# Kernel tuning notes

Measured on AMD Instinct MI355X. Metric: run time of the kernel, lower is better.

Reference implementation:

```python
import jax, jax.numpy as jnp
import numpy as np

B, S, D, H = 4, 2048, 768, 12
HD = D // H  # head dim = 64


def setup_inputs() -> dict:
    key = jax.random.key(0)
    ks = jax.random.split(key, 8)
    w_scale = 0.02
    return {
        "x": jax.random.normal(ks[0], (B, S, D), dtype=jnp.float32),
        "Wq": jax.random.normal(ks[1], (D, D), dtype=jnp.float32) * w_scale,
        "bq": jnp.zeros((D,), dtype=jnp.float32),
        "Wk": jax.random.normal(ks[2], (D, D), dtype=jnp.float32) * w_scale,
        "Wv": jax.random.normal(ks[3], (D, D), dtype=jnp.float32) * w_scale,
        "bv": jnp.zeros((D,), dtype=jnp.float32),
        "Wo": jax.random.normal(ks[4], (D, D), dtype=jnp.float32) * w_scale,
        "bo": jnp.zeros((D,), dtype=jnp.float32),
    }


def reference(x, Wq, bq, Wk, Wv, bv, Wo, bo):
    # Self-attention branch (xa=None, no kv_cache), causal mask enabled.
    q = x @ Wq + bq                       # [B,S,D]; key proj has no bias
    k = x @ Wk
    v = x @ Wv + bv

    def split_heads(t):
        return t.reshape(B, S, H, HD).transpose(0, 2, 1, 3)  # [B,H,S,HD]

    q, k, v = split_heads(q), split_heads(k), split_heads(v)

    scale = float(HD) ** -0.5  # applied once to qk == (hd**-0.25 on q and k)
    qk = jnp.einsum("bhqd,bhkd->bhqk", q, k) * scale  # [B,H,S,S]

    # dynamic causal mask: -inf where kv index > q index
    causal = jnp.where(
        jnp.arange(S)[:, None] < jnp.arange(S)[None, :], -jnp.inf, 0.0
    ).astype(jnp.float32)
    qk = qk + causal

    w = jax.nn.softmax(qk.astype(jnp.float32), axis=-1).astype(q.dtype)
    out = jnp.einsum("bhqk,bhkd->bhqd", w, v)          # [B,H,S,HD]
    out = out.transpose(0, 2, 1, 3).reshape(B, S, D)    # [B,S,D]
    output = out @ Wo + bo
    return output, jax.lax.stop_gradient(qk)
```

## Files before the change

kernel.cpp:

```cpp
#include <hip/hip_runtime.h>
#include <cmath>

#define BB 4
#define SS 2048
#define DD 768
#define HH 12
#define HDD 64
#define MROWS (BB * SS)
#define NHEADS (BB * HH)

#define MASK_SENTINEL (-3.0e38f)

template <bool SPLIT_HEADS>
__global__ __launch_bounds__(256) void gemm768(const float* __restrict__ A,
                                               const float* __restrict__ W,
                                               const float* __restrict__ bias,
                                               float* __restrict__ out) {
    __shared__ float As[16][68];
    __shared__ float Bs[16][68];

    const int tid = threadIdx.x;
    const int tx = tid & 15;
    const int ty = tid >> 4;
    const int m0 = blockIdx.y * 64;
    const int n0 = blockIdx.x * 64;

    const int ar = tid >> 2;
    const int ac4 = (tid & 3) * 4;
    const int br = tid >> 4;
    const int bc4 = (tid & 15) * 4;

    float acc[4][4] = {};

    for (int k0 = 0; k0 < 768; k0 += 16) {
        if (k0 != 0) __syncthreads();
        const float4 av = *reinterpret_cast<const float4*>(
            &A[(size_t)(m0 + ar) * 768 + k0 + ac4]);
        As[ac4 + 0][ar] = av.x;
        As[ac4 + 1][ar] = av.y;
        As[ac4 + 2][ar] = av.z;
        As[ac4 + 3][ar] = av.w;
        *reinterpret_cast<float4*>(&Bs[br][bc4]) =
            *reinterpret_cast<const float4*>(&W[(size_t)(k0 + br) * 768 + n0 + bc4]);
        __syncthreads();

#pragma unroll
        for (int kk = 0; kk < 16; ++kk) {
            const float4 a = *reinterpret_cast<const float4*>(&As[kk][ty * 4]);
            const float4 b = *reinterpret_cast<const float4*>(&Bs[kk][tx * 4]);
            const float af[4] = {a.x, a.y, a.z, a.w};
            const float bf[4] = {b.x, b.y, b.z, b.w};
#pragma unroll
            for (int i = 0; i < 4; ++i)
#pragma unroll
                for (int j = 0; j < 4; ++j)
                    acc[i][j] = fmaf(af[i], bf[j], acc[i][j]);
        }
    }

#pragma unroll
    for (int i = 0; i < 4; ++i) {
        const int m = m0 + ty * 4 + i;
#pragma unroll
        for (int j = 0; j < 4; ++j) {
            const int n = n0 + tx * 4 + j;
            float v = acc[i][j];
            if (bias != nullptr) v += bias[n];
            if (SPLIT_HEADS) {
                const int b = m >> 11;
                const int s = m & 2047;
                const int h = n >> 6;
                const int hd = n & 63;
                out[(((size_t)(b * HH + h)) * SS + s) * HDD + hd] = v;
            } else {
                out[(size_t)m * 768 + n] = v;
            }
        }
    }
}

__global__ __launch_bounds__(256) void attn_flash(const float* __restrict__ q,
                                                  const float* __restrict__ k,
                                                  const float* __restrict__ v,
                                                  float* __restrict__ qk_out,
                                                  float* __restrict__ attn_out) {
    __shared__ float Ks[64][68];
    __shared__ float Vs[64][68];

    const int tid = threadIdx.x;
    const int quarter = tid & 3;
    const int row = tid >> 2;
    const int pair = blockIdx.x;
    const int bh = blockIdx.y;
    const size_t head_base = (size_t)bh * SS * HDD;
    const float scale = 0.125f;
    const int b_idx = bh / HH;
    const int h_idx = bh % HH;

    const int sr = tid >> 2;
    const int scb = (tid & 3) * 16;

#pragma unroll 1
    for (int leg = 0; leg < 2; ++leg) {
        const int tq = (leg == 0) ? (31 - pair) : pair;
        const int q0 = tq * 64;
        const int qr = q0 + row;

        float4 qreg[4];
        {
            const float* qp = q + head_base + (size_t)qr * HDD + quarter * 16;
#pragma unroll
            for (int c = 0; c < 4; ++c)
                qreg[c] = reinterpret_cast<const float4*>(qp)[c];
        }

        float4 o[4];
#pragma unroll
        for (int c = 0; c < 4; ++c) o[c] = make_float4(0.f, 0.f, 0.f, 0.f);
        float m_i = -INFINITY;
        float l_i = 0.0f;

        float* qk_row = qk_out + ((size_t)bh * SS + qr) * SS;

        const int kt_end = tq + 1;

        for (int kt = 0; kt < kt_end; ++kt) {
            __syncthreads();
            {
                const float* kp = k + head_base + (size_t)(kt * 64 + sr) * HDD + scb;
                const float* vp = v + head_base + (size_t)(kt * 64 + sr) * HDD + scb;
#pragma unroll
                for (int i = 0; i < 4; ++i) {
                    *reinterpret_cast<float4*>(&Ks[sr][scb + i * 4]) =
                        reinterpret_cast<const float4*>(kp)[i];
                    *reinterpret_cast<float4*>(&Vs[sr][scb + i * 4]) =
                        reinterpret_cast<const float4*>(vp)[i];
                }
            }
            __syncthreads();

            for (int jc = 0; jc < 64; jc += 16) {
                float sreg[16];
#pragma unroll
                for (int jj = 0; jj < 16; ++jj) {
                    const int j = jc + jj;
                    float acc = 0.f;
#pragma unroll
                    for (int c = 0; c < 4; ++c) {
                        const float4 kv = *reinterpret_cast<const float4*>(
                            &Ks[j][quarter * 16 + c * 4]);
                        acc = fmaf(qreg[c].x, kv.x, acc);
                        acc = fmaf(qreg[c].y, kv.y, acc);
                        acc = fmaf(qreg[c].z, kv.z, acc);
                        acc = fmaf(qreg[c].w, kv.w, acc);
                    }
                    acc += __shfl_xor(acc, 1);
                    acc += __shfl_xor(acc, 2);
                    const int jg = kt * 64 + j;
                    sreg[jj] = (jg > qr) ? -INFINITY : acc * scale;
                }

                {
                    const float w0 = fmaxf(sreg[quarter * 4 + 0], MASK_SENTINEL);
                    const float w1 = fmaxf(sreg[quarter * 4 + 1], MASK_SENTINEL);
                    const float w2 = fmaxf(sreg[quarter * 4 + 2], MASK_SENTINEL);
                    const float w3 = fmaxf(sreg[quarter * 4 + 3], MASK_SENTINEL);
                    *reinterpret_cast<float4*>(&qk_row[kt * 64 + jc + quarter * 4]) =
                        make_float4(w0, w1, w2, w3);
                }

                float mc = sreg[0];
#pragma unroll
                for (int jj = 1; jj < 16; ++jj) mc = fmaxf(mc, sreg[jj]);
                const float m_new = fmaxf(m_i, mc);
                if (m_new != -INFINITY) {
                    const float alpha = __expf(m_i - m_new);
                    float psum = 0.f;
#pragma unroll
                    for (int jj = 0; jj < 16; ++jj) {
                        sreg[jj] = __expf(sreg[jj] - m_new);
                        psum += sreg[jj];
                    }
                    l_i = l_i * alpha + psum;
                    m_i = m_new;
#pragma unroll
                    for (int c = 0; c < 4; ++c) {
                        o[c].x *= alpha;
                        o[c].y *= alpha;
                        o[c].z *= alpha;
                        o[c].w *= alpha;
                    }
#pragma unroll
                    for (int jj = 0; jj < 16; ++jj) {
                        const float p = sreg[jj];
#pragma unroll
                        for (int c = 0; c < 4; ++c) {
                            const float4 vv = *reinterpret_cast<const float4*>(
                                &Vs[jc + jj][quarter * 16 + c * 4]);
                            o[c].x = fmaf(p, vv.x, o[c].x);
                            o[c].y = fmaf(p, vv.y, o[c].y);
                            o[c].z = fmaf(p, vv.z, o[c].z);
                            o[c].w = fmaf(p, vv.w, o[c].w);
                        }
                    }
                }
            }
        }

        const float4 sent4 = make_float4(MASK_SENTINEL, MASK_SENTINEL,
                                         MASK_SENTINEL, MASK_SENTINEL);
        for (int base = kt_end * 64; base < SS; base += 16)
            *reinterpret_cast<float4*>(&qk_row[base + quarter * 4]) = sent4;

        const float inv_l = 1.0f / l_i;
        float* op = attn_out + ((size_t)(b_idx * SS + qr)) * DD + h_idx * HDD +
                    quarter * 16;
#pragma unroll
        for (int c = 0; c < 4; ++c) {
            float4 t = o[c];
            t.x *= inv_l;
            t.y *= inv_l;
            t.z *= inv_l;
            t.w *= inv_l;
            reinterpret_cast<float4*>(op)[c] = t;
        }
    }
}

extern "C" void kernel_launch(void* const* d_in, const int* in_sizes, int n_in,
                              void* d_out, int out_size, void* d_ws, size_t ws_size,
                              hipStream_t stream) {
    const float* x = (const float*)d_in[0];
    const float* Wq = (const float*)d_in[1];
    const float* bq = (const float*)d_in[2];
    const float* Wk = (const float*)d_in[3];
    const float* Wv = (const float*)d_in[4];
    const float* bv = (const float*)d_in[5];
    const float* Wo = (const float*)d_in[6];
    const float* bo = (const float*)d_in[7];

    float* out = (float*)d_out;
    float* qk = out + (size_t)BB * SS * DD;

    const size_t seg = (size_t)BB * SS * DD;
    float* qws = (float*)d_ws;
    float* kws = qws + seg;
    float* vws = qws + 2 * seg;
    float* aws = qws + 3 * seg;

    const dim3 gblk(256);
    const dim3 ggrid(DD / 64, MROWS / 64);

    gemm768<true><<<ggrid, gblk, 0, stream>>>(x, Wq, bq, qws);
    gemm768<true><<<ggrid, gblk, 0, stream>>>(x, Wk, nullptr, kws);
    gemm768<true><<<ggrid, gblk, 0, stream>>>(x, Wv, bv, vws);

    attn_flash<<<dim3(16, NHEADS), dim3(256), 0, stream>>>(qws, kws, vws, qk, aws);

    gemm768<false><<<ggrid, gblk, 0, stream>>>(aws, Wo, bo, out);
}
```

Measured before the change: 2.251 ms.

## Enlarge GEMM register tiles and give each attention thread two query rows

The projection GEMM moves to 128x64 block tiles with an 8x8 register tile per thread, 128 threads per block, register-staged global loads and vectorized epilogue stores. The attention kernel now has each thread handle two query rows over an 8-wide slice of the head dimension, so each K/V shared-memory read is reused for two rows. It also prefetches K/V into registers before the barrier, uses non-temporal stores for the large qk output, and replaces the dead-row branch with selects. Larger per-thread tiles raise register pressure and may reduce occupancy, and the wider shuffle reduction adds a step per score.

```diff
diff --git a/kernel.cpp b/kernel.cpp
--- a/kernel.cpp
+++ b/kernel.cpp
@@ -11,70 +11,92 @@
 
 #define MASK_SENTINEL (-3.0e38f)
 
+typedef float f32x4v __attribute__((ext_vector_type(4)));
+
+__device__ __forceinline__ void nt_store4(float* p, float a, float b, float c,
+                                          float d) {
+    f32x4v t = {a, b, c, d};
+    __builtin_nontemporal_store(t, reinterpret_cast<f32x4v*>(p));
+}
+
 template <bool SPLIT_HEADS>
-__global__ __launch_bounds__(256) void gemm768(const float* __restrict__ A,
+__global__ __launch_bounds__(128) void gemm768(const float* __restrict__ A,
                                                const float* __restrict__ W,
                                                const float* __restrict__ bias,
                                                float* __restrict__ out) {
-    __shared__ float As[16][68];
+    __shared__ float As[16][132];
     __shared__ float Bs[16][68];
 
     const int tid = threadIdx.x;
-    const int tx = tid & 15;
-    const int ty = tid >> 4;
-    const int m0 = blockIdx.y * 64;
+    const int tx = tid & 7;
+    const int ty = tid >> 3;
+    const int m0 = blockIdx.y * 128;
     const int n0 = blockIdx.x * 64;
 
-    const int ar = tid >> 2;
-    const int ac4 = (tid & 3) * 4;
-    const int br = tid >> 4;
-    const int bc4 = (tid & 15) * 4;
-
-    float acc[4][4] = {};
+    const int br = tid >> 3;
+    const int bc = (tid & 7) * 8;
+
+    float acc[8][8] = {};
 
     for (int k0 = 0; k0 < 768; k0 += 16) {
+        float4 av[4];
+        const float* ap = &A[(size_t)(m0 + tid) * 768 + k0];
+#pragma unroll
+        for (int c = 0; c < 4; ++c) av[c] = reinterpret_cast<const float4*>(ap)[c];
+        float4 bv[2];
+        const float* bp = &W[(size_t)(k0 + br) * 768 + n0 + bc];
+        bv[0] = reinterpret_cast<const float4*>(bp)[0];
+        bv[1] = reinterpret_cast<const float4*>(bp)[1];
+
         if (k0 != 0) __syncthreads();
-        const float4 av = *reinterpret_cast<const float4*>(
-            &A[(size_t)(m0 + ar) * 768 + k0 + ac4]);
-        As[ac4 + 0][ar] = av.x;
-        As[ac4 + 1][ar] = av.y;
-        As[ac4 + 2][ar] = av.z;
-        As[ac4 + 3][ar] = av.w;
-        *reinterpret_cast<float4*>(&Bs[br][bc4]) =
-            *reinterpret_cast<const float4*>(&W[(size_t)(k0 + br) * 768 + n0 + bc4]);
+#pragma unroll
+        for (int c = 0; c < 4; ++c) {
+            As[c * 4 + 0][tid] = av[c].x;
+            As[c * 4 + 1][tid] = av[c].y;
+            As[c * 4 + 2][tid] = av[c].z;
+            As[c * 4 + 3][tid] = av[c].w;
+        }
+        *reinterpret_cast<float4*>(&Bs[br][bc]) = bv[0];
+        *reinterpret_cast<float4*>(&Bs[br][bc + 4]) = bv[1];
         __syncthreads();
 
 #pragma unroll
         for (int kk = 0; kk < 16; ++kk) {
-            const float4 a = *reinterpret_cast<const float4*>(&As[kk][ty * 4]);
-            const float4 b = *reinterpret_cast<const float4*>(&Bs[kk][tx * 4]);
-            const float af[4] = {a.x, a.y, a.z, a.w};
-            const float bf[4] = {b.x, b.y, b.z, b.w};
-#pragma unroll
-            for (int i = 0; i < 4; ++i)
-#pragma unroll
-                for (int j = 0; j < 4; ++j)
+            const float4 a0 = *reinterpret_cast<const float4*>(&As[kk][ty * 8]);
+            const float4 a1 = *reinterpret_cast<const float4*>(&As[kk][ty * 8 + 4]);
+            const float4 b0 = *reinterpret_cast<const float4*>(&Bs[kk][tx * 8]);
+            const float4 b1 = *reinterpret_cast<const float4*>(&Bs[kk][tx * 8 + 4]);
+            const float af[8] = {a0.x, a0.y, a0.z, a0.w, a1.x, a1.y, a1.z, a1.w};
+            const float bf[8] = {b0.x, b0.y, b0.z, b0.w, b1.x, b1.y, b1.z, b1.w};
+#pragma unroll
+            for (int i = 0; i < 8; ++i)
+#pragma unroll
+                for (int j = 0; j < 8; ++j)
                     acc[i][j] = fmaf(af[i], bf[j], acc[i][j]);
         }
     }
 
-#pragma unroll
-    for (int i = 0; i < 4; ++i) {
-        const int m = m0 + ty * 4 + i;
-#pragma unroll
-        for (int j = 0; j < 4; ++j) {
-            const int n = n0 + tx * 4 + j;
-            float v = acc[i][j];
-            if (bias != nullptr) v += bias[n];
-            if (SPLIT_HEADS) {
-                const int b = m >> 11;
-                const int s = m & 2047;
-                const int h = n >> 6;
-                const int hd = n & 63;
-                out[(((size_t)(b * HH + h)) * SS + s) * HDD + hd] = v;
-            } else {
-                out[(size_t)m * 768 + n] = v;
-            }
+    float bn[8];
+#pragma unroll
+    for (int j = 0; j < 8; ++j) bn[j] = (bias != nullptr) ? bias[n0 + tx * 8 + j] : 0.f;
+
+    const int h = n0 >> 6;
+#pragma unroll
+    for (int i = 0; i < 8; ++i) {
+        const int m = m0 + ty * 8 + i;
+        float r[8];
+#pragma unroll
+        for (int j = 0; j < 8; ++j) r[j] = acc[i][j] + bn[j];
+        if (SPLIT_HEADS) {
+            const int b = m >> 11;
+            const int s = m & 2047;
+            float* op = &out[(((size_t)(b * HH + h)) * SS + s) * HDD + tx * 8];
+            *reinterpret_cast<float4*>(op) = make_float4(r[0], r[1], r[2], r[3]);
+            *reinterpret_cast<float4*>(op + 4) = make_float4(r[4], r[5], r[6], r[7]);
+        } else {
+            float* op = &out[(size_t)m * 768 + n0 + tx * 8];
+            *reinterpret_cast<float4*>(op) = make_float4(r[0], r[1], r[2], r[3]);
+            *reinterpret_cast<float4*>(op + 4) = make_float4(r[4], r[5], r[6], r[7]);
         }
     }
 }
@@ -88,8 +110,9 @@
     __shared__ float Vs[64][68];
 
     const int tid = threadIdx.x;
-    const int quarter = tid & 3;
-    const int row = tid >> 2;
+    const int oct = tid & 7;
+    const int rg = (tid >> 3) & 31;
+    const int d0 = oct * 8;
     const int pair = blockIdx.x;
     const int bh = blockIdx.y;
     const size_t head_base = (size_t)bh * SS * HDD;
@@ -100,129 +123,190 @@
     const int sr = tid >> 2;
     const int scb = (tid & 3) * 16;
 
+    const int rsel = oct >> 2;
+    const int g = oct & 3;
+
 #pragma unroll 1
     for (int leg = 0; leg < 2; ++leg) {
         const int tq = (leg == 0) ? (31 - pair) : pair;
         const int q0 = tq * 64;
-        const int qr = q0 + row;
-
-        float4 qreg[4];
+        const int qr0 = q0 + rg;
+        const int qr1 = q0 + rg + 32;
+
+        float4 q0reg[2], q1reg[2];
         {
-            const float* qp = q + head_base + (size_t)qr * HDD + quarter * 16;
-#pragma unroll
-            for (int c = 0; c < 4; ++c)
-                qreg[c] = reinterpret_cast<const float4*>(qp)[c];
-        }
-
-        float4 o[4];
-#pragma unroll
-        for (int c = 0; c < 4; ++c) o[c] = make_float4(0.f, 0.f, 0.f, 0.f);
-        float m_i = -INFINITY;
-        float l_i = 0.0f;
-
-        float* qk_row = qk_out + ((size_t)bh * SS + qr) * SS;
+            const float* qp0 = q + head_base + (size_t)qr0 * HDD + d0;
+            const float* qp1 = q + head_base + (size_t)qr1 * HDD + d0;
+            q0reg[0] = reinterpret_cast<const float4*>(qp0)[0];
+            q0reg[1] = reinterpret_cast<const float4*>(qp0)[1];
+            q1reg[0] = reinterpret_cast<const float4*>(qp1)[0];
+            q1reg[1] = reinterpret_cast<const float4*>(qp1)[1];
+        }
+
+        float4 o0[2], o1[2];
+#pragma unroll
+        for (int c = 0; c < 2; ++c) {
+            o0[c] = make_float4(0.f, 0.f, 0.f, 0.f);
+            o1[c] = make_float4(0.f, 0.f, 0.f, 0.f);
+        }
+        float m0i = -INFINITY, l0 = 0.f;
+        float m1i = -INFINITY, l1 = 0.f;
+
+        float* qk_row0 = qk_out + ((size_t)bh * SS + qr0) * SS;
+        float* qk_row1 = qk_out + ((size_t)bh * SS + qr1) * SS;
 
         const int kt_end = tq + 1;
 
         for (int kt = 0; kt < kt_end; ++kt) {
-            __syncthreads();
+            float4 kreg[4], vreg[4];
             {
                 const float* kp = k + head_base + (size_t)(kt * 64 + sr) * HDD + scb;
                 const float* vp = v + head_base + (size_t)(kt * 64 + sr) * HDD + scb;
 #pragma unroll
                 for (int i = 0; i < 4; ++i) {
-                    *reinterpret_cast<float4*>(&Ks[sr][scb + i * 4]) =
-                        reinterpret_cast<const float4*>(kp)[i];
-                    *reinterpret_cast<float4*>(&Vs[sr][scb + i * 4]) =
-                        reinterpret_cast<const float4*>(vp)[i];
+                    kreg[i] = reinterpret_cast<const float4*>(kp)[i];
+                    vreg[i] = reinterpret_cast<const float4*>(vp)[i];
                 }
             }
             __syncthreads();
+#pragma unroll
+            for (int i = 0; i < 4; ++i) {
+                *reinterpret_cast<float4*>(&Ks[sr][scb + i * 4]) = kreg[i];
+                *reinterpret_cast<float4*>(&Vs[sr][scb + i * 4]) = vreg[i];
+            }
+            __syncthreads();
 
             for (int jc = 0; jc < 64; jc += 16) {
-                float sreg[16];
+                float s0[16], s1[16];
 #pragma unroll
                 for (int jj = 0; jj < 16; ++jj) {
                     const int j = jc + jj;
-                    float acc = 0.f;
-#pragma unroll
-                    for (int c = 0; c < 4; ++c) {
-                        const float4 kv = *reinterpret_cast<const float4*>(
-                            &Ks[j][quarter * 16 + c * 4]);
-                        acc = fmaf(qreg[c].x, kv.x, acc);
-                        acc = fmaf(qreg[c].y, kv.y, acc);
-                        acc = fmaf(qreg[c].z, kv.z, acc);
-                        acc = fmaf(qreg[c].w, kv.w, acc);
+                    const float4 kv0 = *reinterpret_cast<const float4*>(&Ks[j][d0]);
+                    const float4 kv1 =
+                        *reinterpret_cast<const float4*>(&Ks[j][d0 + 4]);
+                    float a0 = 0.f, a1 = 0.f;
+                    a0 = fmaf(q0reg[0].x, kv0.x, a0);
+                    a0 = fmaf(q0reg[0].y, kv0.y, a0);
+                    a0 = fmaf(q0reg[0].z, kv0.z, a0);
+                    a0 = fmaf(q0reg[0].w, kv0.w, a0);
+                    a0 = fmaf(q0reg[1].x, kv1.x, a0);
+                    a0 = fmaf(q0reg[1].y, kv1.y, a0);
+                    a0 = fmaf(q0reg[1].z, kv1.z, a0);
+                    a0 = fmaf(q0reg[1].w, kv1.w, a0);
+                    a1 = fmaf(q1reg[0].x, kv0.x, a1);
+                    a1 = fmaf(q1reg[0].y, kv0.y, a1);
+                    a1 = fmaf(q1reg[0].z, kv0.z, a1);
+                    a1 = fmaf(q1reg[0].w, kv0.w, a1);
+                    a1 = fmaf(q1reg[1].x, kv1.x, a1);
+                    a1 = fmaf(q1reg[1].y, kv1.y, a1);
+                    a1 = fmaf(q1reg[1].z, kv1.z, a1);
+                    a1 = fmaf(q1reg[1].w, kv1.w, a1);
+                    a0 += __shfl_xor(a0, 1);
+                    a0 += __shfl_xor(a0, 2);
+                    a0 += __shfl_xor(a0, 4);
+                    a1 += __shfl_xor(a1, 1);
+                    a1 += __shfl_xor(a1, 2);
+                    a1 += __shfl_xor(a1, 4);
+                    const int jg = kt * 64 + j;
+                    s0[jj] = (jg > qr0) ? -INFINITY : a0 * scale;
+                    s1[jj] = (jg > qr1) ? -INFINITY : a1 * scale;
+                }
+
+                {
+                    float w[4];
+#pragma unroll
+                    for (int t = 0; t < 4; ++t) {
+                        const float x01 = (g & 1) ? s0[4 + t] : s0[t];
+                        const float x23 = (g & 1) ? s0[12 + t] : s0[8 + t];
+                        const float xs = (g & 2) ? x23 : x01;
+                        const float y01 = (g & 1) ? s1[4 + t] : s1[t];
+                        const float y23 = (g & 1) ? s1[12 + t] : s1[8 + t];
+                        const float ys = (g & 2) ? y23 : y01;
+                        w[t] = fmaxf(rsel ? ys : xs, MASK_SENTINEL);
                     }
-                    acc += __shfl_xor(acc, 1);
-                    acc += __shfl_xor(acc, 2);
-                    const int jg = kt * 64 + j;
-                    sreg[jj] = (jg > qr) ? -INFINITY : acc * scale;
-                }
-
-                {
-                    const float w0 = fmaxf(sreg[quarter * 4 + 0], MASK_SENTINEL);
-                    const float w1 = fmaxf(sreg[quarter * 4 + 1], MASK_SENTINEL);
-                    const float w2 = fmaxf(sreg[quarter * 4 + 2], MASK_SENTINEL);
-                    const float w3 = fmaxf(sreg[quarter * 4 + 3], MASK_SENTINEL);
-                    *reinterpret_cast<float4*>(&qk_row[kt * 64 + jc + quarter * 4]) =
-                        make_float4(w0, w1, w2, w3);
-                }
-
-                float mc = sreg[0];
-#pragma unroll
-                for (int jj = 1; jj < 16; ++jj) mc = fmaxf(mc, sreg[jj]);
-                const float m_new = fmaxf(m_i, mc);
-                if (m_new != -INFINITY) {
-                    const float alpha = __expf(m_i - m_new);
-                    float psum = 0.f;
-#pragma unroll
-                    for (int jj = 0; jj < 16; ++jj) {
-                        sreg[jj] = __expf(sreg[jj] - m_new);
-                        psum += sreg[jj];
-                    }
-                    l_i = l_i * alpha + psum;
-                    m_i = m_new;
-#pragma unroll
-                    for (int c = 0; c < 4; ++c) {
-                        o[c].x *= alpha;
-                        o[c].y *= alpha;
-                        o[c].z *= alpha;
-                        o[c].w *= alpha;
-                    }
-#pragma unroll
-                    for (int jj = 0; jj < 16; ++jj) {
-                        const float p = sreg[jj];
-#pragma unroll
-                        for (int c = 0; c < 4; ++c) {
-                            const float4 vv = *reinterpret_cast<const float4*>(
-                                &Vs[jc + jj][quarter * 16 + c * 4]);
-                            o[c].x = fmaf(p, vv.x, o[c].x);
-                            o[c].y = fmaf(p, vv.y, o[c].y);
-                            o[c].z = fmaf(p, vv.z, o[c].z);
-                            o[c].w = fmaf(p, vv.w, o[c].w);
-                        }
-                    }
+                    float* dst = (rsel ? qk_row1 : qk_row0) + kt * 64 + jc + g * 4;
+                    nt_store4(dst, w[0], w[1], w[2], w[3]);
+                }
+
+                float mc0 = s0[0], mc1 = s1[0];
+#pragma unroll
+                for (int jj = 1; jj < 16; ++jj) {
+                    mc0 = fmaxf(mc0, s0[jj]);
+                    mc1 = fmaxf(mc1, s1[jj]);
+                }
+                const float mn0 = fmaxf(m0i, mc0);
+                const float mn1 = fmaxf(m1i, mc1);
+                const bool dead0 = (mn0 == -INFINITY);
+                const bool dead1 = (mn1 == -INFINITY);
+                const float alpha0 = dead0 ? 1.f : __expf(m0i - mn0);
+                const float alpha1 = dead1 ? 1.f : __expf(m1i - mn1);
+                const float sub0 = dead0 ? 0.f : mn0;
+                const float sub1 = dead1 ? 0.f : mn1;
+                m0i = mn0;
+                m1i = mn1;
+                float ps0 = 0.f, ps1 = 0.f;
+#pragma unroll
+                for (int jj = 0; jj < 16; ++jj) {
+                    s0[jj] = __expf(s0[jj] - sub0);
+                    s1[jj] = __expf(s1[jj] - sub1);
+                    ps0 += s0[jj];
+                    ps1 += s1[jj];
+                }
+                l0 = l0 * alpha0 + ps0;
+                l1 = l1 * alpha1 + ps1;
+#pragma unroll
+                for (int c = 0; c < 2; ++c) {
+                    o0[c].x *= alpha0; o0[c].y *= alpha0;
+                    o0[c].z *= alpha0; o0[c].w *= alpha0;
+                    o1[c].x *= alpha1; o1[c].y *= alpha1;
+                    o1[c].z *= alpha1; o1[c].w *= alpha1;
+                }
+#pragma unroll
+                for (int jj = 0; jj < 16; ++jj) {
+                    const float4 vv0 =
+                        *reinterpret_cast<const float4*>(&Vs[jc + jj][d0]);
+                    const float4 vv1 =
+                        *reinterpret_cast<const float4*>(&Vs[jc + jj][d0 + 4]);
+                    const float p0 = s0[jj];
+                    const float p1 = s1[jj];
+                    o0[0].x = fmaf(p0, vv0.x, o0[0].x);
+                    o0[0].y = fmaf(p0, vv0.y, o0[0].y);
+                    o0[0].z = fmaf(p0, vv0.z, o0[0].z);
+                    o0[0].w = fmaf(p0, vv0.w, o0[0].w);
+                    o0[1].x = fmaf(p0, vv1.x, o0[1].x);
+                    o0[1].y = fmaf(p0, vv1.y, o0[1].y);
+                    o0[1].z = fmaf(p0, vv1.z, o0[1].z);
+                    o0[1].w = fmaf(p0, vv1.w, o0[1].w);
+                    o1[0].x = fmaf(p1, vv0.x, o1[0].x);
+                    o1[0].y = fmaf(p1, vv0.y, o1[0].y);
+                    o1[0].z = fmaf(p1, vv0.z, o1[0].z);
+                    o1[0].w = fmaf(p1, vv0.w, o1[0].w);
+                    o1[1].x = fmaf(p1, vv1.x, o1[1].x);
+                    o1[1].y = fmaf(p1, vv1.y, o1[1].y);
+                    o1[1].z = fmaf(p1, vv1.z, o1[1].z);
+                    o1[1].w = fmaf(p1, vv1.w, o1[1].w);
                 }
             }
         }
 
-        const float4 sent4 = make_float4(MASK_SENTINEL, MASK_SENTINEL,
-                                         MASK_SENTINEL, MASK_SENTINEL);
-        for (int base = kt_end * 64; base < SS; base += 16)
-            *reinterpret_cast<float4*>(&qk_row[base + quarter * 4]) = sent4;
-
-        const float inv_l = 1.0f / l_i;
-        float* op = attn_out + ((size_t)(b_idx * SS + qr)) * DD + h_idx * HDD +
-                    quarter * 16;
-#pragma unroll
-        for (int c = 0; c < 4; ++c) {
-            float4 t = o[c];
-            t.x *= inv_l;
-            t.y *= inv_l;
-            t.z *= inv_l;
-            t.w *= inv_l;
-            reinterpret_cast<float4*>(op)[c] = t;
+        for (int base = kt_end * 64; base < SS; base += 32) {
+            nt_store4(&qk_row0[base + oct * 4], MASK_SENTINEL, MASK_SENTINEL,
+                      MASK_SENTINEL, MASK_SENTINEL);
+            nt_store4(&qk_row1[base + oct * 4], MASK_SENTINEL, MASK_SENTINEL,
+                      MASK_SENTINEL, MASK_SENTINEL);
+        }
+
+        const float inv0 = 1.0f / l0;
+        const float inv1 = 1.0f / l1;
+        float* op0 = attn_out + ((size_t)(b_idx * SS + qr0)) * DD + h_idx * HDD + d0;
+        float* op1 = attn_out + ((size_t)(b_idx * SS + qr1)) * DD + h_idx * HDD + d0;
+#pragma unroll
+        for (int c = 0; c < 2; ++c) {
+            float4 t0 = o0[c], t1 = o1[c];
+            t0.x *= inv0; t0.y *= inv0; t0.z *= inv0; t0.w *= inv0;
+            t1.x *= inv1; t1.y *= inv1; t1.z *= inv1; t1.w *= inv1;
+            reinterpret_cast<float4*>(op0)[c] = t0;
+            reinterpret_cast<float4*>(op1)[c] = t1;
         }
     }
 }
@@ -248,8 +332,8 @@
     float* vws = qws + 2 * seg;
     float* aws = qws + 3 * seg;
 
-    const dim3 gblk(256);
-    const dim3 ggrid(DD / 64, MROWS / 64);
+    const dim3 gblk(128);
+    const dim3 ggrid(DD / 64, MROWS / 128);
 
     gemm768<true><<<ggrid, gblk, 0, stream>>>(x, Wq, bq, qws);
     gemm768<true><<<ggrid, gblk, 0, stream>>>(x, Wk, nullptr, kws);
```

Result: slower. 2.772 ms (+23.1%).
